# Performance work log

Measured on AMD Instinct MI355X. Metric: run time of the kernel, lower is better.

The kernel has to match this reference:

```python
import jax, jax.numpy as jnp
import numpy as np

H = 8
D_MODEL = 512
D_K = D_MODEL // H


def setup_inputs() -> dict:
    key = jax.random.key(0)
    ks = jax.random.split(key, 12)
    B, S = 4, 2048
    scale = 1.0 / np.sqrt(D_MODEL)
    inp = {
        "query": jax.random.normal(ks[0], (B, S, D_MODEL), jnp.float32),
        "key": jax.random.normal(ks[1], (B, S, D_MODEL), jnp.float32),
        "value": jax.random.normal(ks[2], (B, S, D_MODEL), jnp.float32),
        "mask": jnp.ones((B, 1, S), jnp.int32),
        "Wq": jax.random.normal(ks[3], (D_MODEL, D_MODEL), jnp.float32) * scale,
        "bq": jax.random.normal(ks[4], (D_MODEL,), jnp.float32) * 0.01,
        "Wk": jax.random.normal(ks[5], (D_MODEL, D_MODEL), jnp.float32) * scale,
        "bk": jax.random.normal(ks[6], (D_MODEL,), jnp.float32) * 0.01,
        "Wv": jax.random.normal(ks[7], (D_MODEL, D_MODEL), jnp.float32) * scale,
        "bv": jax.random.normal(ks[8], (D_MODEL,), jnp.float32) * 0.01,
        "Wo": jax.random.normal(ks[9], (D_MODEL, D_MODEL), jnp.float32) * scale,
        "bo": jax.random.normal(ks[10], (D_MODEL,), jnp.float32) * 0.01,
    }
    return inp


def reference(query, key, value, mask, Wq, bq, Wk, bk, Wv, bv, Wo, bo):
    B, S, _ = query.shape

    def proj(x, W, b):
        # [B,S,D] -> [B,H,S,d_k]
        y = jnp.einsum('bsd,ed->bse', x, W) + b  # torch Linear: x @ W.T + b
        return y.reshape(B, S, H, D_K).transpose(0, 2, 1, 3)

    q = proj(query, Wq, bq)
    k = proj(key, Wk, bk)
    v = proj(value, Wv, bv)

    scores = jnp.einsum('bhqd,bhkd->bhqk', q, k) / jnp.sqrt(jnp.float32(D_K))
    m = mask[:, None, :, :]  # [B,1,1,S]
    scores = jnp.where(m == 0, jnp.float32(-1e9), scores)
    p_attn = jax.nn.softmax(scores, axis=-1)  # dropout is identity in eval
    x = jnp.einsum('bhqk,bhkd->bhqd', p_attn, v)
    x = x.transpose(0, 2, 1, 3).reshape(B, S, D_MODEL)
    return jnp.einsum('bsd,ed->bse', x, Wo) + bo
```

## Files before the change

kernel.cpp:

```cpp
#include <hip/hip_runtime.h>
#include <hip/hip_bf16.h>

#define H 8
#define DMODEL 512
#define DK 64
#define BATCH 4
#define SEQ 2048
#define M_TOTAL (BATCH*SEQ)

typedef short bf16x8 __attribute__((ext_vector_type(8)));
typedef float f32x4 __attribute__((ext_vector_type(4)));

__device__ __forceinline__ unsigned short f2bf(float f) {
    unsigned int u = __builtin_bit_cast(unsigned int, f);
    u += 0x7FFFu + ((u >> 16) & 1u);
    return (unsigned short)(u >> 16);
}

__device__ __forceinline__ unsigned int pack_bf2(float a, float b) {
    unsigned int r;
    asm("v_cvt_pk_bf16_f32 %0, %1, %2" : "=v"(r) : "v"(a), "v"(b));
    return r;
}

__device__ __forceinline__ float exp2_fast(float x) {
    float r;
    asm("v_exp_f32 %0, %1" : "=v"(r) : "v"(x));
    return r;
}

__global__ __launch_bounds__(256) void gemm_qkv(
    const float* __restrict__ query, const float* __restrict__ key_,
    const float* __restrict__ value,
    const float* __restrict__ Wq, const float* __restrict__ bq,
    const float* __restrict__ Wk, const float* __restrict__ bk,
    const float* __restrict__ Wv, const float* __restrict__ bv,
    unsigned short* __restrict__ Qh, unsigned short* __restrict__ Kh,
    unsigned short* __restrict__ Vt)
{
    const int z = blockIdx.z;
    const float* A    = (z == 0) ? query : (z == 1) ? key_ : value;
    const float* W    = (z == 0) ? Wq : (z == 1) ? Wk : Wv;
    const float* bias = (z == 0) ? bq : (z == 1) ? bk : bv;
    unsigned short* out = (z == 0) ? Qh : (z == 1) ? Kh : Vt;

    const int m0 = blockIdx.x * 128;
    const int n0 = blockIdx.y * 64;
    const int tid = threadIdx.x;
    const int lane = tid & 63;
    const int w = tid >> 6;
    const int g = lane >> 4, qi = lane & 15;
    const int wm = w >> 1, wn = w & 1;

    __shared__ unsigned short Alds[128 * 40];
    __shared__ unsigned short Blds[64 * 40];

    f32x4 acc[4][2];
    #pragma unroll
    for (int i = 0; i < 4; i++)
        #pragma unroll
        for (int j = 0; j < 2; j++) acc[i][j] = f32x4{0.f, 0.f, 0.f, 0.f};

    float4 aA[4], bA[2], aB[4], bB[2];

    auto ld = [&](float4 (&ar)[4], float4 (&br)[2], int k0) {
        #pragma unroll
        for (int i = 0; i < 4; i++) { int idx = tid + i * 256;
            ar[i] = *(const float4*)(A + (size_t)(m0 + (idx >> 3)) * 512 + k0 + (idx & 7) * 4); }
        #pragma unroll
        for (int i = 0; i < 2; i++) { int idx = tid + i * 256;
            br[i] = *(const float4*)(W + (size_t)(n0 + (idx >> 3)) * 512 + k0 + (idx & 7) * 4); }
    };
    auto st = [&](float4 (&ar)[4], float4 (&br)[2]) {
        #pragma unroll
        for (int i = 0; i < 4; i++) { int idx = tid + i * 256;
            uint2 p; p.x = pack_bf2(ar[i].x, ar[i].y); p.y = pack_bf2(ar[i].z, ar[i].w);
            *(uint2*)(Alds + (idx >> 3) * 40 + (idx & 7) * 4) = p; }
        #pragma unroll
        for (int i = 0; i < 2; i++) { int idx = tid + i * 256;
            uint2 p; p.x = pack_bf2(br[i].x, br[i].y); p.y = pack_bf2(br[i].z, br[i].w);
            *(uint2*)(Blds + (idx >> 3) * 40 + (idx & 7) * 4) = p; }
    };
    auto tile = [&]() {
        bf16x8 af[4], bf[2];
        #pragma unroll
        for (int mt = 0; mt < 4; mt++)
            af[mt] = *(const bf16x8*)(Alds + (wm * 64 + mt * 16 + qi) * 40 + g * 8);
        #pragma unroll
        for (int nt = 0; nt < 2; nt++)
            bf[nt] = *(const bf16x8*)(Blds + (wn * 32 + nt * 16 + qi) * 40 + g * 8);
        #pragma unroll
        for (int mt = 0; mt < 4; mt++)
            #pragma unroll
            for (int nt = 0; nt < 2; nt++)
                acc[mt][nt] = __builtin_amdgcn_mfma_f32_16x16x32_bf16(af[mt], bf[nt], acc[mt][nt], 0, 0, 0);
    };

    ld(aA, bA, 0);
    for (int k0 = 0; k0 < 512; k0 += 64) {
        __syncthreads();
        st(aA, bA);
        ld(aB, bB, k0 + 32);
        __syncthreads();
        tile();
        __syncthreads();
        st(aB, bB);
        if (k0 + 64 < 512) ld(aA, bA, k0 + 64);
        __syncthreads();
        tile();
    }

    #pragma unroll
    for (int mt = 0; mt < 4; mt++) {
        int mbase = m0 + wm * 64 + mt * 16 + g * 4;
        #pragma unroll
        for (int nt = 0; nt < 2; nt++) {
            int n = n0 + wn * 32 + nt * 16 + qi;
            float bv = bias[n];
            int h = n >> 6, dk = n & 63;
            if (z == 2) {
                int b = mbase >> 11, s = mbase & 2047;
                uint2 pk;
                pk.x = pack_bf2(acc[mt][nt][0] + bv, acc[mt][nt][1] + bv);
                pk.y = pack_bf2(acc[mt][nt][2] + bv, acc[mt][nt][3] + bv);
                *(uint2*)(out + ((size_t)(b * H + h) * 64 + dk) * SEQ + s) = pk;
            } else {
                float sc = (z == 0) ? 0.18033688011112042f : 1.0f;
                #pragma unroll
                for (int r = 0; r < 4; r++) {
                    int m = mbase + r;
                    int b = m >> 11, s = m & 2047;
                    out[((size_t)(b * H + h) * SEQ + s) * 64 + dk] = f2bf((acc[mt][nt][r] + bv) * sc);
                }
            }
        }
    }
}

__global__ __launch_bounds__(256) void gemm_o(
    const unsigned short* __restrict__ Xa, const float* __restrict__ W,
    const float* __restrict__ bias, float* __restrict__ out)
{
    const int m0 = blockIdx.x * 128;
    const int n0 = blockIdx.y * 64;
    const int tid = threadIdx.x;
    const int lane = tid & 63;
    const int w = tid >> 6;
    const int g = lane >> 4, qi = lane & 15;
    const int wm = w >> 1, wn = w & 1;

    __shared__ unsigned short Alds[128 * 40];
    __shared__ unsigned short Blds[64 * 40];

    f32x4 acc[4][2];
    #pragma unroll
    for (int i = 0; i < 4; i++)
        #pragma unroll
        for (int j = 0; j < 2; j++) acc[i][j] = f32x4{0.f, 0.f, 0.f, 0.f};

    bf16x8 aA[2], aB[2];
    float4 bA[2], bB[2];

    auto ld = [&](bf16x8 (&ar)[2], float4 (&br)[2], int k0) {
        #pragma unroll
        for (int i = 0; i < 2; i++) { int idx = tid + i * 256;
            ar[i] = *(const bf16x8*)(Xa + (size_t)(m0 + (idx >> 2)) * 512 + k0 + (idx & 3) * 8); }
        #pragma unroll
        for (int i = 0; i < 2; i++) { int idx = tid + i * 256;
            br[i] = *(const float4*)(W + (size_t)(n0 + (idx >> 3)) * 512 + k0 + (idx & 7) * 4); }
    };
    auto st = [&](bf16x8 (&ar)[2], float4 (&br)[2]) {
        #pragma unroll
        for (int i = 0; i < 2; i++) { int idx = tid + i * 256;
            *(bf16x8*)(Alds + (idx >> 2) * 40 + (idx & 3) * 8) = ar[i]; }
        #pragma unroll
        for (int i = 0; i < 2; i++) { int idx = tid + i * 256;
            uint2 p; p.x = pack_bf2(br[i].x, br[i].y); p.y = pack_bf2(br[i].z, br[i].w);
            *(uint2*)(Blds + (idx >> 3) * 40 + (idx & 7) * 4) = p; }
    };
    auto tile = [&]() {
        bf16x8 af[4], bf[2];
        #pragma unroll
        for (int mt = 0; mt < 4; mt++)
            af[mt] = *(const bf16x8*)(Alds + (wm * 64 + mt * 16 + qi) * 40 + g * 8);
        #pragma unroll
        for (int nt = 0; nt < 2; nt++)
            bf[nt] = *(const bf16x8*)(Blds + (wn * 32 + nt * 16 + qi) * 40 + g * 8);
        #pragma unroll
        for (int mt = 0; mt < 4; mt++)
            #pragma unroll
            for (int nt = 0; nt < 2; nt++)
                acc[mt][nt] = __builtin_amdgcn_mfma_f32_16x16x32_bf16(af[mt], bf[nt], acc[mt][nt], 0, 0, 0);
    };

    ld(aA, bA, 0);
    for (int k0 = 0; k0 < 512; k0 += 64) {
        __syncthreads();
        st(aA, bA);
        ld(aB, bB, k0 + 32);
        __syncthreads();
        tile();
        __syncthreads();
        st(aB, bB);
        if (k0 + 64 < 512) ld(aA, bA, k0 + 64);
        __syncthreads();
        tile();
    }

    #pragma unroll
    for (int mt = 0; mt < 4; mt++) {
        int mbase = m0 + wm * 64 + mt * 16 + g * 4;
        #pragma unroll
        for (int nt = 0; nt < 2; nt++) {
            int n = n0 + wn * 32 + nt * 16 + qi;
            float bv = bias[n];
            #pragma unroll
            for (int r = 0; r < 4; r++)
                out[(size_t)(mbase + r) * 512 + n] = acc[mt][nt][r] + bv;
        }
    }
}

__global__ __launch_bounds__(256) void attn_kernel(
    const unsigned short* __restrict__ Qh,
    const unsigned short* __restrict__ Kh,
    const unsigned short* __restrict__ Vt,
    const int* __restrict__ mask,
    unsigned short* __restrict__ Xattn)
{
    const int tid = threadIdx.x;
    const int lane = tid & 63;
    const int w = tid >> 6;
    const int g = lane >> 4;
    const int qi = lane & 15;
    const int s3 = qi & 7;

    const int bid = blockIdx.x;
    const int xcd = bid & 7;
    const int slot = bid >> 3;
    const int bh = xcd * 4 + (slot >> 4);
    const int q0 = (slot & 15) * 128;
    const int b = bh >> 3;

    __shared__ unsigned short Klds[2][64 * 64];
    __shared__ unsigned short Vlds[2][64 * 64];
    __shared__ unsigned short Plds[4][32 * 64];

    bf16x8 qf[2][2];
    #pragma unroll
    for (int f = 0; f < 2; f++) {
        const unsigned short* Qbase =
            Qh + ((size_t)bh * SEQ + q0 + w * 32 + f * 16 + qi) * 64 + g * 8;
        qf[f][0] = *(const bf16x8*)(Qbase);
        qf[f][1] = *(const bf16x8*)(Qbase + 32);
    }

    f32x4 acc_o[2][4];
    #pragma unroll
    for (int f = 0; f < 2; f++)
        #pragma unroll
        for (int dt = 0; dt < 4; dt++) acc_o[f][dt] = f32x4{0.f, 0.f, 0.f, 0.f};
    float l_lane[2] = {0.f, 0.f};

    const unsigned char* Kbh = (const unsigned char*)(Kh + (size_t)bh * SEQ * 64);
    const unsigned char* Vbh = (const unsigned char*)(Vt + (size_t)bh * 64 * SEQ);
    const int* maskb = mask + b * SEQ;

    const int klane = ((lane >> 3) << 7)  + (((lane & 7) ^ (lane >> 3)) << 4);
    const int vlane = ((lane >> 3) << 12) + (((lane & 7) ^ (lane >> 3)) << 4);

    const int rb0 = qi * 128 + ((g ^ s3) << 4);
    const unsigned char* PldsB = (const unsigned char*)&Plds[w][0];
    const int pw0 = qi * 128 + (((g >> 1) ^ s3) << 4) + ((g & 1) << 3);

    auto stage = [&](int t, int buf) {
        const unsigned char* ks = Kbh + t * 8192 + klane;
        const unsigned char* vs = Vbh + t * 128 + vlane;
        unsigned char* kd = (unsigned char*)&Klds[buf][0];
        unsigned char* vd = (unsigned char*)&Vlds[buf][0];
        #pragma unroll
        for (int j = 0; j < 2; j++) {
            const int c = w + 4 * j;
            __builtin_amdgcn_global_load_lds(
                (const __attribute__((address_space(1))) unsigned int*)(ks + c * 1024),
                (__attribute__((address_space(3))) unsigned int*)(kd + c * 1024), 16, 0, 0);
            __builtin_amdgcn_global_load_lds(
                (const __attribute__((address_space(1))) unsigned int*)(vs + c * 32768),
                (__attribute__((address_space(3))) unsigned int*)(vd + c * 1024), 16, 0, 0);
        }
    };

    auto compute = [&](int t, int buf) {
        const int kv0 = t << 6;
        const unsigned char* KB = (const unsigned char*)&Klds[buf][0];
        const unsigned char* VB = (const unsigned char*)&Vlds[buf][0];

        const unsigned long long mb = __ballot(maskb[kv0 + lane] != 0);

        f32x4 sacc[2][4];
        #pragma unroll
        for (int nt = 0; nt < 4; nt++) {
            bf16x8 kf0 = *(const bf16x8*)(KB + (rb0 ^ 0)  + nt * 2048);
            bf16x8 kf1 = *(const bf16x8*)(KB + (rb0 ^ 64) + nt * 2048);
            #pragma unroll
            for (int f = 0; f < 2; f++) {
                f32x4 sa = f32x4{0.f, 0.f, 0.f, 0.f};
                sa = __builtin_amdgcn_mfma_f32_16x16x32_bf16(kf0, qf[f][0], sa, 0, 0, 0);
                sa = __builtin_amdgcn_mfma_f32_16x16x32_bf16(kf1, qf[f][1], sa, 0, 0, 0);
                sacc[f][nt] = sa;
            }
        }

        if (mb != ~0ull) {
            #pragma unroll
            for (int f = 0; f < 2; f++)
                #pragma unroll
                for (int nt = 0; nt < 4; nt++)
                    #pragma unroll
                    for (int r = 0; r < 4; r++) {
                        int kvl = nt * 16 + g * 4 + r;
                        if (!((mb >> kvl) & 1ull)) sacc[f][nt][r] = -1e9f;
                    }
        }

        #pragma unroll
        for (int f = 0; f < 2; f++) {
            #pragma unroll
            for (int nt = 0; nt < 4; nt++) {
                float p0 = exp2_fast(sacc[f][nt][0]);
                float p1 = exp2_fast(sacc[f][nt][1]);
                float p2 = exp2_fast(sacc[f][nt][2]);
                float p3 = exp2_fast(sacc[f][nt][3]);
                l_lane[f] += (p0 + p1) + (p2 + p3);
                uint2 pk;
                pk.x = pack_bf2(p0, p1);
                pk.y = pack_bf2(p2, p3);
                *(uint2*)((unsigned char*)&Plds[w][0] + f * 2048 +
                          (pw0 ^ (nt << 5))) = pk;
            }
        }

        #pragma unroll
        for (int kt = 0; kt < 2; kt++) {
            bf16x8 pf0 = *(const bf16x8*)(PldsB + 0    + (rb0 ^ (kt << 6)));
            bf16x8 pf1 = *(const bf16x8*)(PldsB + 2048 + (rb0 ^ (kt << 6)));
            #pragma unroll
            for (int dt = 0; dt < 4; dt++) {
                bf16x8 vf = *(const bf16x8*)(VB + (rb0 ^ (kt << 6)) + dt * 2048);
                acc_o[0][dt] = __builtin_amdgcn_mfma_f32_16x16x32_bf16(vf, pf0, acc_o[0][dt], 0, 0, 0);
                acc_o[1][dt] = __builtin_amdgcn_mfma_f32_16x16x32_bf16(vf, pf1, acc_o[1][dt], 0, 0, 0);
            }
        }
    };

    stage(0, 0);
    __syncthreads();
    #pragma unroll 1
    for (int t = 0; t < 32; t += 2) {
        stage(t + 1, 1);
        compute(t, 0);
        __syncthreads();
        if (t + 2 < 32) stage(t + 2, 0);
        compute(t + 1, 1);
        __syncthreads();
    }

    const int h = bh & 7;
    #pragma unroll
    for (int f = 0; f < 2; f++) {
        float l = l_lane[f];
        l += __shfl_xor(l, 16);
        l += __shfl_xor(l, 32);
        const float inv = 1.0f / l;
        const int s = q0 + w * 32 + f * 16 + qi;
        size_t base = ((size_t)b * SEQ + s) * 512 + h * 64;
        #pragma unroll
        for (int dt = 0; dt < 4; dt++) {
            uint2 o;
            o.x = pack_bf2(acc_o[f][dt][0] * inv, acc_o[f][dt][1] * inv);
            o.y = pack_bf2(acc_o[f][dt][2] * inv, acc_o[f][dt][3] * inv);
            *(uint2*)(Xattn + base + dt * 16 + g * 4) = o;
        }
    }
}

extern "C" void kernel_launch(void* const* d_in, const int* in_sizes, int n_in,
                              void* d_out, int out_size, void* d_ws, size_t ws_size,
                              hipStream_t stream)
{
    const float* query = (const float*)d_in[0];
    const float* key_  = (const float*)d_in[1];
    const float* value = (const float*)d_in[2];
    const int*   mask  = (const int*)d_in[3];
    const float* Wq = (const float*)d_in[4];
    const float* bq = (const float*)d_in[5];
    const float* Wk = (const float*)d_in[6];
    const float* bk = (const float*)d_in[7];
    const float* Wv = (const float*)d_in[8];
    const float* bv = (const float*)d_in[9];
    const float* Wo = (const float*)d_in[10];
    const float* bo = (const float*)d_in[11];

    unsigned short* Qh = (unsigned short*)d_ws;
    unsigned short* Kh = Qh + (size_t)M_TOTAL * DMODEL;
    unsigned short* Vt = Kh + (size_t)M_TOTAL * DMODEL;
    unsigned short* Xa = Vt + (size_t)M_TOTAL * DMODEL;

    dim3 thr(256);
    hipLaunchKernelGGL(gemm_qkv, dim3(64, 8, 3), thr, 0, stream,
                       query, key_, value, Wq, bq, Wk, bk, Wv, bv, Qh, Kh, Vt);
    hipLaunchKernelGGL(attn_kernel, dim3(512), thr, 0, stream, Qh, Kh, Vt, mask, Xa);
    hipLaunchKernelGGL(gemm_o, dim3(64, 8), thr, 0, stream, Xa, Wo, bo, (float*)d_out);
}
```

Measured before the change: 95.37 us.

## Widen QKV GEMM tile, shrink attention blocks to 128 threads, add MFMA priority

The QKV projection GEMM now computes 128x128 tiles instead of 128x64, which halves the number of A-tile reloads at the cost of more accumulator registers. The attention kernel switches to 128-thread blocks covering 64 queries each, launched over twice as many blocks, and its double-buffer loop is simplified to one stage per iteration. The attention kernel also hoists V fragment loads ahead of the softmax and interleaves the P write/read with the PV MFMAs per fragment. s_setprio is wrapped around the MFMA sections in all GEMM and attention loops to favour matrix issue across waves.

Result: slower. 113.5 us (+19.0%).

```diff
diff --git a/kernel.cpp b/kernel.cpp
--- a/kernel.cpp
+++ b/kernel.cpp
@@ -45,7 +45,7 @@
     unsigned short* out = (z == 0) ? Qh : (z == 1) ? Kh : Vt;
 
     const int m0 = blockIdx.x * 128;
-    const int n0 = blockIdx.y * 64;
+    const int n0 = blockIdx.y * 128;
     const int tid = threadIdx.x;
     const int lane = tid & 63;
     const int w = tid >> 6;
@@ -53,47 +53,49 @@
     const int wm = w >> 1, wn = w & 1;
 
     __shared__ unsigned short Alds[128 * 40];
-    __shared__ unsigned short Blds[64 * 40];
-
-    f32x4 acc[4][2];
+    __shared__ unsigned short Blds[128 * 40];
+
+    f32x4 acc[4][4];
     #pragma unroll
     for (int i = 0; i < 4; i++)
         #pragma unroll
-        for (int j = 0; j < 2; j++) acc[i][j] = f32x4{0.f, 0.f, 0.f, 0.f};
-
-    float4 aA[4], bA[2], aB[4], bB[2];
-
-    auto ld = [&](float4 (&ar)[4], float4 (&br)[2], int k0) {
+        for (int j = 0; j < 4; j++) acc[i][j] = f32x4{0.f, 0.f, 0.f, 0.f};
+
+    float4 aA[4], bA[4], aB[4], bB[4];
+
+    auto ld = [&](float4 (&ar)[4], float4 (&br)[4], int k0) {
         #pragma unroll
         for (int i = 0; i < 4; i++) { int idx = tid + i * 256;
             ar[i] = *(const float4*)(A + (size_t)(m0 + (idx >> 3)) * 512 + k0 + (idx & 7) * 4); }
         #pragma unroll
-        for (int i = 0; i < 2; i++) { int idx = tid + i * 256;
+        for (int i = 0; i < 4; i++) { int idx = tid + i * 256;
             br[i] = *(const float4*)(W + (size_t)(n0 + (idx >> 3)) * 512 + k0 + (idx & 7) * 4); }
     };
-    auto st = [&](float4 (&ar)[4], float4 (&br)[2]) {
+    auto st = [&](float4 (&ar)[4], float4 (&br)[4]) {
         #pragma unroll
         for (int i = 0; i < 4; i++) { int idx = tid + i * 256;
             uint2 p; p.x = pack_bf2(ar[i].x, ar[i].y); p.y = pack_bf2(ar[i].z, ar[i].w);
             *(uint2*)(Alds + (idx >> 3) * 40 + (idx & 7) * 4) = p; }
         #pragma unroll
-        for (int i = 0; i < 2; i++) { int idx = tid + i * 256;
+        for (int i = 0; i < 4; i++) { int idx = tid + i * 256;
             uint2 p; p.x = pack_bf2(br[i].x, br[i].y); p.y = pack_bf2(br[i].z, br[i].w);
             *(uint2*)(Blds + (idx >> 3) * 40 + (idx & 7) * 4) = p; }
     };
     auto tile = [&]() {
-        bf16x8 af[4], bf[2];
+        bf16x8 af[4], bf[4];
         #pragma unroll
         for (int mt = 0; mt < 4; mt++)
             af[mt] = *(const bf16x8*)(Alds + (wm * 64 + mt * 16 + qi) * 40 + g * 8);
         #pragma unroll
-        for (int nt = 0; nt < 2; nt++)
-            bf[nt] = *(const bf16x8*)(Blds + (wn * 32 + nt * 16 + qi) * 40 + g * 8);
+        for (int nt = 0; nt < 4; nt++)
+            bf[nt] = *(const bf16x8*)(Blds + (wn * 64 + nt * 16 + qi) * 40 + g * 8);
+        __builtin_amdgcn_s_setprio(1);
         #pragma unroll
         for (int mt = 0; mt < 4; mt++)
             #pragma unroll
-            for (int nt = 0; nt < 2; nt++)
+            for (int nt = 0; nt < 4; nt++)
                 acc[mt][nt] = __builtin_amdgcn_mfma_f32_16x16x32_bf16(af[mt], bf[nt], acc[mt][nt], 0, 0, 0);
+        __builtin_amdgcn_s_setprio(0);
     };
 
     ld(aA, bA, 0);
@@ -114,8 +116,8 @@
     for (int mt = 0; mt < 4; mt++) {
         int mbase = m0 + wm * 64 + mt * 16 + g * 4;
         #pragma unroll
-        for (int nt = 0; nt < 2; nt++) {
-            int n = n0 + wn * 32 + nt * 16 + qi;
+        for (int nt = 0; nt < 4; nt++) {
+            int n = n0 + wn * 64 + nt * 16 + qi;
             float bv = bias[n];
             int h = n >> 6, dk = n & 63;
             if (z == 2) {
@@ -186,11 +188,13 @@
         #pragma unroll
         for (int nt = 0; nt < 2; nt++)
             bf[nt] = *(const bf16x8*)(Blds + (wn * 32 + nt * 16 + qi) * 40 + g * 8);
+        __builtin_amdgcn_s_setprio(1);
         #pragma unroll
         for (int mt = 0; mt < 4; mt++)
             #pragma unroll
             for (int nt = 0; nt < 2; nt++)
                 acc[mt][nt] = __builtin_amdgcn_mfma_f32_16x16x32_bf16(af[mt], bf[nt], acc[mt][nt], 0, 0, 0);
+        __builtin_amdgcn_s_setprio(0);
     };
 
     ld(aA, bA, 0);
@@ -221,7 +225,7 @@
     }
 }
 
-__global__ __launch_bounds__(256) void attn_kernel(
+__global__ __launch_bounds__(128) void attn_kernel(
     const unsigned short* __restrict__ Qh,
     const unsigned short* __restrict__ Kh,
     const unsigned short* __restrict__ Vt,
@@ -238,13 +242,13 @@
     const int bid = blockIdx.x;
     const int xcd = bid & 7;
     const int slot = bid >> 3;
-    const int bh = xcd * 4 + (slot >> 4);
-    const int q0 = (slot & 15) * 128;
+    const int bh = xcd * 4 + (slot >> 5);
+    const int q0 = (slot & 31) * 64;
     const int b = bh >> 3;
 
     __shared__ unsigned short Klds[2][64 * 64];
     __shared__ unsigned short Vlds[2][64 * 64];
-    __shared__ unsigned short Plds[4][32 * 64];
+    __shared__ unsigned short Plds[2][16 * 64];
 
     bf16x8 qf[2][2];
     #pragma unroll
@@ -270,8 +274,8 @@
     const int vlane = ((lane >> 3) << 12) + (((lane & 7) ^ (lane >> 3)) << 4);
 
     const int rb0 = qi * 128 + ((g ^ s3) << 4);
-    const unsigned char* PldsB = (const unsigned char*)&Plds[w][0];
     const int pw0 = qi * 128 + (((g >> 1) ^ s3) << 4) + ((g & 1) << 3);
+    unsigned char* Pw = (unsigned char*)&Plds[w][0];
 
     auto stage = [&](int t, int buf) {
         const unsigned char* ks = Kbh + t * 8192 + klane;
@@ -279,8 +283,8 @@
         unsigned char* kd = (unsigned char*)&Klds[buf][0];
         unsigned char* vd = (unsigned char*)&Vlds[buf][0];
         #pragma unroll
-        for (int j = 0; j < 2; j++) {
-            const int c = w + 4 * j;
+        for (int j = 0; j < 4; j++) {
+            const int c = w + 2 * j;
             __builtin_amdgcn_global_load_lds(
                 (const __attribute__((address_space(1))) unsigned int*)(ks + c * 1024),
                 (__attribute__((address_space(3))) unsigned int*)(kd + c * 1024), 16, 0, 0);
@@ -295,12 +299,11 @@
         const unsigned char* KB = (const unsigned char*)&Klds[buf][0];
         const unsigned char* VB = (const unsigned char*)&Vlds[buf][0];
 
-        const unsigned long long mb = __ballot(maskb[kv0 + lane] != 0);
-
         f32x4 sacc[2][4];
+        __builtin_amdgcn_s_setprio(1);
         #pragma unroll
         for (int nt = 0; nt < 4; nt++) {
-            bf16x8 kf0 = *(const bf16x8*)(KB + (rb0 ^ 0)  + nt * 2048);
+            bf16x8 kf0 = *(const bf16x8*)(KB + rb0 + nt * 2048);
             bf16x8 kf1 = *(const bf16x8*)(KB + (rb0 ^ 64) + nt * 2048);
             #pragma unroll
             for (int f = 0; f < 2; f++) {
@@ -310,7 +313,9 @@
                 sacc[f][nt] = sa;
             }
         }
-
+        __builtin_amdgcn_s_setprio(0);
+
+        const unsigned long long mb = __ballot(maskb[kv0 + lane] != 0);
         if (mb != ~0ull) {
             #pragma unroll
             for (int f = 0; f < 2; f++)
@@ -322,6 +327,13 @@
                         if (!((mb >> kvl) & 1ull)) sacc[f][nt][r] = -1e9f;
                     }
         }
+
+        bf16x8 vf[8];
+        #pragma unroll
+        for (int kt = 0; kt < 2; kt++)
+            #pragma unroll
+            for (int dt = 0; dt < 4; dt++)
+                vf[kt * 4 + dt] = *(const bf16x8*)(VB + (rb0 ^ (kt << 6)) + dt * 2048);
 
         #pragma unroll
         for (int f = 0; f < 2; f++) {
@@ -335,33 +347,27 @@
                 uint2 pk;
                 pk.x = pack_bf2(p0, p1);
                 pk.y = pack_bf2(p2, p3);
-                *(uint2*)((unsigned char*)&Plds[w][0] + f * 2048 +
-                          (pw0 ^ (nt << 5))) = pk;
+                *(uint2*)(Pw + (pw0 ^ (nt << 5))) = pk;
             }
-        }
-
-        #pragma unroll
-        for (int kt = 0; kt < 2; kt++) {
-            bf16x8 pf0 = *(const bf16x8*)(PldsB + 0    + (rb0 ^ (kt << 6)));
-            bf16x8 pf1 = *(const bf16x8*)(PldsB + 2048 + (rb0 ^ (kt << 6)));
+            bf16x8 pf0 = *(const bf16x8*)(Pw + rb0);
+            bf16x8 pf1 = *(const bf16x8*)(Pw + (rb0 ^ 64));
+            __builtin_amdgcn_s_setprio(1);
             #pragma unroll
             for (int dt = 0; dt < 4; dt++) {
-                bf16x8 vf = *(const bf16x8*)(VB + (rb0 ^ (kt << 6)) + dt * 2048);
-                acc_o[0][dt] = __builtin_amdgcn_mfma_f32_16x16x32_bf16(vf, pf0, acc_o[0][dt], 0, 0, 0);
-                acc_o[1][dt] = __builtin_amdgcn_mfma_f32_16x16x32_bf16(vf, pf1, acc_o[1][dt], 0, 0, 0);
+                acc_o[f][dt] = __builtin_amdgcn_mfma_f32_16x16x32_bf16(vf[dt],     pf0, acc_o[f][dt], 0, 0, 0);
+                acc_o[f][dt] = __builtin_amdgcn_mfma_f32_16x16x32_bf16(vf[4 + dt], pf1, acc_o[f][dt], 0, 0, 0);
             }
+            __builtin_amdgcn_s_setprio(0);
         }
     };
 
     stage(0, 0);
     __syncthreads();
     #pragma unroll 1
-    for (int t = 0; t < 32; t += 2) {
-        stage(t + 1, 1);
-        compute(t, 0);
-        __syncthreads();
-        if (t + 2 < 32) stage(t + 2, 0);
-        compute(t + 1, 1);
+    for (int t = 0; t < 32; ++t) {
+        const int buf = t & 1;
+        if (t + 1 < 32) stage(t + 1, buf ^ 1);
+        compute(t, buf);
         __syncthreads();
     }
 
@@ -406,9 +412,8 @@
     unsigned short* Vt = Kh + (size_t)M_TOTAL * DMODEL;
     unsigned short* Xa = Vt + (size_t)M_TOTAL * DMODEL;
 
-    dim3 thr(256);
-    hipLaunchKernelGGL(gemm_qkv, dim3(64, 8, 3), thr, 0, stream,
+    hipLaunchKernelGGL(gemm_qkv, dim3(64, 4, 3), dim3(256), 0, stream,
                        query, key_, value, Wq, bq, Wk, bk, Wv, bv, Qh, Kh, Vt);
-    hipLaunchKernelGGL(attn_kernel, dim3(512), thr, 0, stream, Qh, Kh, Vt, mask, Xa);
-    hipLaunchKernelGGL(gemm_o, dim3(64, 8), thr, 0, stream, Xa, Wo, bo, (float*)d_out);
-}
+    hipLaunchKernelGGL(attn_kernel, dim3(1024), dim3(128), 0, stream, Qh, Kh, Vt, mask, Xa);
+    hipLaunchKernelGGL(gemm_o, dim3(64, 8), dim3(256), 0, stream, Xa, Wo, bo, (float*)d_out);
+}
```
